# Kernel tuning notes

Hardware: AMD Instinct MI355X
Metric: run time of the kernel (lower is better)

The kernel has to match this reference:

```python
import jax, jax.numpy as jnp
import numpy as np

DIM = 512
HEAD_DIM = 32
NUM_HEADS = DIM // HEAD_DIM
SCALE = HEAD_DIM ** -0.5


def setup_inputs() -> dict:
    key = jax.random.key(0)
    k1, k2, k3 = jax.random.split(key, 3)
    B, H, W, C = 8, 32, 32, DIM
    x = jax.random.normal(k1, (B, H, W, C), dtype=jnp.float32)
    w_qkv = jax.random.normal(k2, (C, 3 * C), dtype=jnp.float32) * (C ** -0.5)
    w_proj = jax.random.normal(k3, (C, C), dtype=jnp.float32) * (C ** -0.5)
    b_proj = jnp.zeros((C,), dtype=jnp.float32)
    return {"x": x, "w_qkv": w_qkv, "w_proj": w_proj, "b_proj": b_proj}


def reference(x, w_qkv, w_proj, b_proj):
    B, H, W, C = x.shape
    N = H * W
    xt = x.reshape(B, N, C)
    qkv = xt @ w_qkv                       # [B, N, 3C]
    qkv = qkv.reshape(B, N, 3, NUM_HEADS, HEAD_DIM)
    qkv = jnp.transpose(qkv, (2, 0, 3, 1, 4))  # [3, B, heads, N, head_dim]
    q, k, v = qkv[0], qkv[1], qkv[2]
    attn = jnp.einsum('bhid,bhjd->bhij', q * SCALE, k)  # [B, heads, N, N]
    attn = jax.nn.softmax(attn, axis=-1)
    out = jnp.einsum('bhij,bhjd->bhid', attn, v)        # [B, heads, N, head_dim]
    out = jnp.transpose(out, (0, 2, 1, 3)).reshape(B, N, C)
    out = out @ w_proj + b_proj
    return out.reshape(B, H, W, C)
```

## Files before the change

### kernel.cpp

```cpp
#include <hip/hip_runtime.h>
#include <hip/hip_bf16.h>

typedef __bf16 bf16x8 __attribute__((ext_vector_type(8)));
typedef __bf16 bf16x4v __attribute__((ext_vector_type(4)));
typedef __bf16 bf16x2v __attribute__((ext_vector_type(2)));
typedef float  f32x4  __attribute__((ext_vector_type(4)));
typedef float  f32x16 __attribute__((ext_vector_type(16)));

#define NB 8
#define NTOK 1024
#define CDIM 512
#define NHEAD 16
#define HDIM 32
#define ATT_SCALE 0.17677669529663687f
#define LOG2E 1.4426950408889634f
#define QSCALE2 (ATT_SCALE * LOG2E)
#define NEGM2 (-12.0f * LOG2E)

struct __align__(8) bf4pack { __hip_bfloat16 x, y, z, w; };

__global__ __launch_bounds__(256)
void k_f32_to_bf16(const float* __restrict__ in, __hip_bfloat16* __restrict__ out, int n4) {
  int i = blockIdx.x * blockDim.x + threadIdx.x;
  if (i >= n4) return;
  float4 v = reinterpret_cast<const float4*>(in)[i];
  bf16x4v o = {(__bf16)v.x, (__bf16)v.y, (__bf16)v.z, (__bf16)v.w};
  reinterpret_cast<bf16x4v*>(out)[i] = o;
}

__global__ __launch_bounds__(256)
void k_transpose_bf16(const float* __restrict__ w, __hip_bfloat16* __restrict__ wt,
                      int K, int N) {
  __shared__ float tile[32][33];
  const int n0 = blockIdx.x * 32, k0 = blockIdx.y * 32;
  const int tx = threadIdx.x, ty = threadIdx.y;
  #pragma unroll
  for (int r = ty; r < 32; r += 8) tile[r][tx] = w[(size_t)(k0 + r) * N + n0 + tx];
  __syncthreads();
  #pragma unroll
  for (int r = ty; r < 32; r += 8)
    wt[(size_t)(n0 + r) * K + k0 + tx] = __float2bfloat16(tile[tx][r]);
}

__device__ __forceinline__ void gload_lds16(const void* g, void* l) {
  __builtin_amdgcn_global_load_lds(
      (const __attribute__((address_space(1))) unsigned int*)g,
      (__attribute__((address_space(3))) unsigned int*)l, 16, 0, 0);
}

template <int MODE>
__global__ __launch_bounds__(256, 2)
void gemm128(const __hip_bfloat16* __restrict__ A,
             const __hip_bfloat16* __restrict__ Bt,
             __hip_bfloat16* __restrict__ Qb,
             __hip_bfloat16* __restrict__ Kb,
             __hip_bfloat16* __restrict__ Vtb,
             float* __restrict__ outF,
             const float* __restrict__ bias,
             int mtiles, int ntiles) {
  __shared__ __hip_bfloat16 As[2][128 * 32];
  __shared__ __hip_bfloat16 Bs[2][128 * 32];

  const int t = threadIdx.x;
  const int wid = t >> 6, lane = t & 63;
  const int wr = wid >> 1, wc = wid & 1;
  const int lrow = lane & 15, lk8 = (lane >> 4) * 8;

  const int bid = blockIdx.x;
  const int chunk = (mtiles * ntiles) >> 3;
  const int wg = (bid & 7) * chunk + (bid >> 3);
  const int bm = (wg / ntiles) * 128;
  const int bn = (wg % ntiles) * 128;

  const bool swapped = (MODE == 1) || (bn < 1024);

  const f32x4 fzero = {0.f, 0.f, 0.f, 0.f};
  f32x4 acc[4][4];
  #pragma unroll
  for (int m = 0; m < 4; ++m)
    #pragma unroll
    for (int n = 0; n < 4; ++n) acc[m][n] = fzero;

  auto stage = [&](int buf, int kt) {
    #pragma unroll
    for (int p = 0; p < 2; ++p) {
      const int c = p * 256 + t;
      const int row = c >> 2;
      const int kof = (c & 3) * 8;
      gload_lds16(A + (size_t)(bm + row) * CDIM + kt * 32 + kof,
                  &As[buf][(p * 256 + (t >> 6) * 64) * 8]);
      gload_lds16(Bt + (size_t)(bn + row) * CDIM + kt * 32 + kof,
                  &Bs[buf][(p * 256 + (t >> 6) * 64) * 8]);
    }
  };

  stage(0, 0);
  const int NKT = CDIM / 32;
  for (int kt = 0; kt < NKT; ++kt) {
    __syncthreads();
    if (kt + 1 < NKT) stage((kt + 1) & 1, kt + 1);
    const int bi = kt & 1;
    bf16x8 af[4], bfv[4];
    #pragma unroll
    for (int m = 0; m < 4; ++m)
      af[m] = *reinterpret_cast<const bf16x8*>(&As[bi][(wr * 64 + m * 16 + lrow) * 32 + lk8]);
    #pragma unroll
    for (int n = 0; n < 4; ++n)
      bfv[n] = *reinterpret_cast<const bf16x8*>(&Bs[bi][(wc * 64 + n * 16 + lrow) * 32 + lk8]);
    if (swapped) {
      #pragma unroll
      for (int m = 0; m < 4; ++m)
        #pragma unroll
        for (int n = 0; n < 4; ++n)
          acc[m][n] = __builtin_amdgcn_mfma_f32_16x16x32_bf16(bfv[n], af[m], acc[m][n], 0, 0, 0);
    } else {
      #pragma unroll
      for (int m = 0; m < 4; ++m)
        #pragma unroll
        for (int n = 0; n < 4; ++n)
          acc[m][n] = __builtin_amdgcn_mfma_f32_16x16x32_bf16(af[m], bfv[n], acc[m][n], 0, 0, 0);
    }
  }

  if constexpr (MODE == 0) {
    if (swapped) {
      const float sc = (bn < 512) ? QSCALE2 : 1.0f;
      __hip_bfloat16* dst = (bn < 512) ? Qb : Kb;
      #pragma unroll
      for (int m = 0; m < 4; ++m) {
        #pragma unroll
        for (int n = 0; n < 4; ++n) {
          const int gm = bm + wr * 64 + m * 16 + lrow;
          const int gn0 = bn + wc * 64 + n * 16 + (lane >> 4) * 4;
          const int r = gn0 & 511;
          const int hh = r >> 5, d0 = r & 31;
          const int bb = gm >> 10, tok = gm & 1023;
          const int ph = bb * NHEAD + hh;
          bf16x4v pk = {(__bf16)(acc[m][n][0] * sc), (__bf16)(acc[m][n][1] * sc),
                        (__bf16)(acc[m][n][2] * sc), (__bf16)(acc[m][n][3] * sc)};
          *reinterpret_cast<bf16x4v*>(&dst[((size_t)ph * NTOK + tok) * HDIM + d0]) = pk;
        }
      }
    } else {
      #pragma unroll
      for (int m = 0; m < 4; ++m) {
        #pragma unroll
        for (int n = 0; n < 4; ++n) {
          const int gm0 = bm + wr * 64 + m * 16 + (lane >> 4) * 4;
          const int gn = bn + wc * 64 + n * 16 + lrow;
          const int r = gn & 511;
          const int hh = r >> 5, d = r & 31;
          const int bb = gm0 >> 10, tok0 = gm0 & 1023;
          const int ph = bb * NHEAD + hh;
          bf16x4v pk = {(__bf16)acc[m][n][0], (__bf16)acc[m][n][1],
                        (__bf16)acc[m][n][2], (__bf16)acc[m][n][3]};
          *reinterpret_cast<bf16x4v*>(&Vtb[((size_t)ph * HDIM + d) * NTOK + tok0]) = pk;
        }
      }
    }
  } else {
    float4 bias4[4];
    #pragma unroll
    for (int n = 0; n < 4; ++n)
      bias4[n] = *reinterpret_cast<const float4*>(&bias[bn + wc * 64 + n * 16 + (lane >> 4) * 4]);
    #pragma unroll
    for (int m = 0; m < 4; ++m) {
      #pragma unroll
      for (int n = 0; n < 4; ++n) {
        const int gm = bm + wr * 64 + m * 16 + lrow;
        const int gn0 = bn + wc * 64 + n * 16 + (lane >> 4) * 4;
        float4 w;
        w.x = acc[m][n][0] + bias4[n].x;
        w.y = acc[m][n][1] + bias4[n].y;
        w.z = acc[m][n][2] + bias4[n].z;
        w.w = acc[m][n][3] + bias4[n].w;
        *reinterpret_cast<float4*>(&outF[(size_t)gm * CDIM + gn0]) = w;
      }
    }
  }
}

__device__ __forceinline__ unsigned pk2(float a, float b) {
  bf16x2v t = {(__bf16)a, (__bf16)b};
  return __builtin_bit_cast(unsigned, t);
}

union B32x4 { unsigned u[4]; bf16x8 v; };

__global__ __launch_bounds__(256, 4)
void k_attn(const __hip_bfloat16* __restrict__ Q,
            const __hip_bfloat16* __restrict__ K,
            const __hip_bfloat16* __restrict__ Vt,
            __hip_bfloat16* __restrict__ out) {
  const int wid = threadIdx.x >> 6, lane = threadIdx.x & 63;
  const int pair = blockIdx.x & 127;
  const int qblk = blockIdx.x >> 7;
  const int b = pair >> 4, h = pair & 15;
  const int q0 = qblk * 128 + wid * 32;
  const int lq = lane & 31, hi = lane >> 5;

  const size_t pb = (size_t)pair * NTOK * HDIM;
  const bf16x8 qf0 = *reinterpret_cast<const bf16x8*>(&Q[pb + (size_t)(q0 + lq) * HDIM + hi * 8]);
  const bf16x8 qf1 = *reinterpret_cast<const bf16x8*>(&Q[pb + (size_t)(q0 + lq) * HDIM + 16 + hi * 8]);

  f32x16 o;
  #pragma unroll
  for (int r = 0; r < 16; ++r) o[r] = 0.f;
  float l_r = 0.f;

  const __hip_bfloat16* Kp = &K[pb + (size_t)lq * HDIM + hi * 8];
  const __hip_bfloat16* Vp = &Vt[(size_t)pair * HDIM * NTOK + (size_t)lq * NTOK + hi * 8];

  bf16x8 kc0 = *reinterpret_cast<const bf16x8*>(Kp);
  bf16x8 kc1 = *reinterpret_cast<const bf16x8*>(Kp + 16);

  for (int t = 0; t < 32; ++t) {
    const int tn = (t < 31) ? t + 1 : 31;
    const bf16x8 kn0 = *reinterpret_cast<const bf16x8*>(Kp + (size_t)tn * 32 * HDIM);
    const bf16x8 kn1 = *reinterpret_cast<const bf16x8*>(Kp + (size_t)tn * 32 * HDIM + 16);
    const bf16x8 vf0 = *reinterpret_cast<const bf16x8*>(Vp + t * 32);
    const bf16x8 vf1 = *reinterpret_cast<const bf16x8*>(Vp + t * 32 + 16);

    f32x16 s;
    #pragma unroll
    for (int r = 0; r < 16; ++r) s[r] = NEGM2;
    s = __builtin_amdgcn_mfma_f32_32x32x16_bf16(kc0, qf0, s, 0, 0, 0);
    s = __builtin_amdgcn_mfma_f32_32x32x16_bf16(kc1, qf1, s, 0, 0, 0);

    float p[16];
    #pragma unroll
    for (int r = 0; r < 16; ++r) p[r] = __builtin_amdgcn_exp2f(s[r]);
    {
      const float a0 = p[0] + p[1], a1 = p[2] + p[3], a2 = p[4] + p[5], a3 = p[6] + p[7];
      const float a4 = p[8] + p[9], a5 = p[10] + p[11], a6 = p[12] + p[13], a7 = p[14] + p[15];
      const float b0 = a0 + a1, b1 = a2 + a3, b2 = a4 + a5, b3 = a6 + a7;
      l_r += (b0 + b1) + (b2 + b3);
    }

    {
      unsigned pA = pk2(p[0], p[1]), pB = pk2(p[2], p[3]);
      unsigned pC = pk2(p[4], p[5]), pD = pk2(p[6], p[7]);
      asm("v_permlane32_swap_b32 %0, %1" : "+v"(pA), "+v"(pC));
      asm("v_permlane32_swap_b32 %0, %1" : "+v"(pB), "+v"(pD));
      B32x4 f; f.u[0] = pA; f.u[1] = pB; f.u[2] = pC; f.u[3] = pD;
      o = __builtin_amdgcn_mfma_f32_32x32x16_bf16(vf0, f.v, o, 0, 0, 0);
    }
    {
      unsigned pA = pk2(p[8], p[9]), pB = pk2(p[10], p[11]);
      unsigned pC = pk2(p[12], p[13]), pD = pk2(p[14], p[15]);
      asm("v_permlane32_swap_b32 %0, %1" : "+v"(pA), "+v"(pC));
      asm("v_permlane32_swap_b32 %0, %1" : "+v"(pB), "+v"(pD));
      B32x4 f; f.u[0] = pA; f.u[1] = pB; f.u[2] = pC; f.u[3] = pD;
      o = __builtin_amdgcn_mfma_f32_32x32x16_bf16(vf1, f.v, o, 0, 0, 0);
    }
    kc0 = kn0; kc1 = kn1;
  }

  l_r += __shfl_xor(l_r, 32, 64);
  const float rinv = 1.0f / l_r;
  __hip_bfloat16* orow = &out[((size_t)b * NTOK + q0 + lq) * CDIM + h * HDIM];
  #pragma unroll
  for (int g = 0; g < 4; ++g) {
    bf16x4v w = {(__bf16)(o[4 * g + 0] * rinv), (__bf16)(o[4 * g + 1] * rinv),
                 (__bf16)(o[4 * g + 2] * rinv), (__bf16)(o[4 * g + 3] * rinv)};
    *reinterpret_cast<bf16x4v*>(orow + 8 * g + 4 * hi) = w;
  }
}

extern "C" void kernel_launch(void* const* d_in, const int* in_sizes, int n_in,
                              void* d_out, int out_size, void* d_ws, size_t ws_size,
                              hipStream_t stream) {
  (void)in_sizes; (void)n_in; (void)out_size; (void)ws_size;
  const float* x      = (const float*)d_in[0];
  const float* w_qkv  = (const float*)d_in[1];
  const float* w_proj = (const float*)d_in[2];
  const float* b_proj = (const float*)d_in[3];
  float* out = (float*)d_out;

  char* ws = (char*)d_ws;
  __hip_bfloat16* xb     = (__hip_bfloat16*)(ws);
  __hip_bfloat16* attnO  = xb;
  __hip_bfloat16* wqkvT  = (__hip_bfloat16*)(ws + 8388608);
  __hip_bfloat16* wprojT = (__hip_bfloat16*)(ws + 9961472);
  __hip_bfloat16* Qb     = (__hip_bfloat16*)(ws + 10485760);
  __hip_bfloat16* Kb     = (__hip_bfloat16*)(ws + 18874368);
  __hip_bfloat16* Vtb    = (__hip_bfloat16*)(ws + 27262976);

  k_f32_to_bf16<<<4096, 256, 0, stream>>>(x, xb, (NB * NTOK * CDIM) / 4);
  k_transpose_bf16<<<dim3(1536 / 32, 512 / 32), dim3(32, 8), 0, stream>>>(w_qkv, wqkvT, 512, 1536);
  k_transpose_bf16<<<dim3(512 / 32, 512 / 32), dim3(32, 8), 0, stream>>>(w_proj, wprojT, 512, 512);

  gemm128<0><<<64 * 12, 256, 0, stream>>>(xb, wqkvT, Qb, Kb, Vtb, nullptr, nullptr, 64, 12);
  k_attn<<<128 * 8, 256, 0, stream>>>(Qb, Kb, Vtb, attnO);
  gemm128<1><<<64 * 4, 256, 0, stream>>>(attnO, wprojT, nullptr, nullptr, nullptr, out, b_proj, 64, 4);
}
```

Baseline: 169.0 us.

## Software-pipeline attention QK^T with exp and merge weight transposes into one launch

The attention loop is restructured so the QK^T MFMAs for the next key tile are issued before the exp2 and PV MFMAs of the current tile. K is prefetched two tiles ahead and V one ahead, with ping-pong register sets. This is meant to hide MFMA latency and the dependency between the score computation and the softmax/PV work. The two weight-transpose kernels are also fused into a single launch to save one kernel launch, at the cost of extra live registers in the attention kernel.

```diff
diff --git a/kernel.cpp b/kernel.cpp
--- a/kernel.cpp
+++ b/kernel.cpp
@@ -17,8 +17,6 @@
 #define QSCALE2 (ATT_SCALE * LOG2E)
 #define NEGM2 (-12.0f * LOG2E)
 
-struct __align__(8) bf4pack { __hip_bfloat16 x, y, z, w; };
-
 __global__ __launch_bounds__(256)
 void k_f32_to_bf16(const float* __restrict__ in, __hip_bfloat16* __restrict__ out, int n4) {
   int i = blockIdx.x * blockDim.x + threadIdx.x;
@@ -29,17 +27,22 @@
 }
 
 __global__ __launch_bounds__(256)
-void k_transpose_bf16(const float* __restrict__ w, __hip_bfloat16* __restrict__ wt,
-                      int K, int N) {
+void k_transpose_w(const float* __restrict__ wqkv, const float* __restrict__ wproj,
+                   __hip_bfloat16* __restrict__ wqkvT, __hip_bfloat16* __restrict__ wprojT) {
   __shared__ float tile[32][33];
   const int n0 = blockIdx.x * 32, k0 = blockIdx.y * 32;
   const int tx = threadIdx.x, ty = threadIdx.y;
-  #pragma unroll
-  for (int r = ty; r < 32; r += 8) tile[r][tx] = w[(size_t)(k0 + r) * N + n0 + tx];
+  const bool isP = (n0 >= 1536);
+  const float* src = isP ? wproj : wqkv;
+  __hip_bfloat16* dst = isP ? wprojT : wqkvT;
+  const int N = isP ? 512 : 1536;
+  const int nc = isP ? n0 - 1536 : n0;
+  #pragma unroll
+  for (int r = ty; r < 32; r += 8) tile[r][tx] = src[(size_t)(k0 + r) * N + nc + tx];
   __syncthreads();
   #pragma unroll
   for (int r = ty; r < 32; r += 8)
-    wt[(size_t)(n0 + r) * K + k0 + tx] = __float2bfloat16(tile[tx][r]);
+    dst[(size_t)(nc + r) * 512 + k0 + tx] = __float2bfloat16(tile[tx][r]);
 }
 
 __device__ __forceinline__ void gload_lds16(const void* g, void* l) {
@@ -203,57 +206,70 @@
   const bf16x8 qf0 = *reinterpret_cast<const bf16x8*>(&Q[pb + (size_t)(q0 + lq) * HDIM + hi * 8]);
   const bf16x8 qf1 = *reinterpret_cast<const bf16x8*>(&Q[pb + (size_t)(q0 + lq) * HDIM + 16 + hi * 8]);
 
-  f32x16 o;
-  #pragma unroll
-  for (int r = 0; r < 16; ++r) o[r] = 0.f;
+  f32x16 o, negm;
+  #pragma unroll
+  for (int r = 0; r < 16; ++r) { o[r] = 0.f; negm[r] = NEGM2; }
   float l_r = 0.f;
 
   const __hip_bfloat16* Kp = &K[pb + (size_t)lq * HDIM + hi * 8];
   const __hip_bfloat16* Vp = &Vt[(size_t)pair * HDIM * NTOK + (size_t)lq * NTOK + hi * 8];
 
-  bf16x8 kc0 = *reinterpret_cast<const bf16x8*>(Kp);
-  bf16x8 kc1 = *reinterpret_cast<const bf16x8*>(Kp + 16);
-
-  for (int t = 0; t < 32; ++t) {
-    const int tn = (t < 31) ? t + 1 : 31;
-    const bf16x8 kn0 = *reinterpret_cast<const bf16x8*>(Kp + (size_t)tn * 32 * HDIM);
-    const bf16x8 kn1 = *reinterpret_cast<const bf16x8*>(Kp + (size_t)tn * 32 * HDIM + 16);
-    const bf16x8 vf0 = *reinterpret_cast<const bf16x8*>(Vp + t * 32);
-    const bf16x8 vf1 = *reinterpret_cast<const bf16x8*>(Vp + t * 32 + 16);
-
-    f32x16 s;
-    #pragma unroll
-    for (int r = 0; r < 16; ++r) s[r] = NEGM2;
-    s = __builtin_amdgcn_mfma_f32_32x32x16_bf16(kc0, qf0, s, 0, 0, 0);
-    s = __builtin_amdgcn_mfma_f32_32x32x16_bf16(kc1, qf1, s, 0, 0, 0);
-
-    float p[16];
-    #pragma unroll
-    for (int r = 0; r < 16; ++r) p[r] = __builtin_amdgcn_exp2f(s[r]);
+  bf16x8 kA0, kA1, kB0, kB1, vA0, vA1, vB0, vB1;
+  f32x16 sA, sB;
+  {
+    const bf16x8 t0 = *reinterpret_cast<const bf16x8*>(Kp);
+    const bf16x8 t1 = *reinterpret_cast<const bf16x8*>(Kp + 16);
+    kA0 = *reinterpret_cast<const bf16x8*>(Kp + 1024);
+    kA1 = *reinterpret_cast<const bf16x8*>(Kp + 1024 + 16);
+    vA0 = *reinterpret_cast<const bf16x8*>(Vp);
+    vA1 = *reinterpret_cast<const bf16x8*>(Vp + 16);
+    sA = __builtin_amdgcn_mfma_f32_32x32x16_bf16(t0, qf0, negm, 0, 0, 0);
+    sA = __builtin_amdgcn_mfma_f32_32x32x16_bf16(t1, qf1, sA, 0, 0, 0);
+  }
+
+  auto body = [&](int t, f32x16& s_cur, f32x16& s_next,
+                  bf16x8& ka0, bf16x8& ka1, bf16x8& kb0, bf16x8& kb1,
+                  bf16x8& va0, bf16x8& va1, bf16x8& vb0, bf16x8& vb1) {
+    const int tk = (t + 2 < 32) ? t + 2 : 31;
+    const int tv = (t + 1 < 32) ? t + 1 : 31;
+    kb0 = *reinterpret_cast<const bf16x8*>(Kp + (size_t)tk * 1024);
+    kb1 = *reinterpret_cast<const bf16x8*>(Kp + (size_t)tk * 1024 + 16);
+    vb0 = *reinterpret_cast<const bf16x8*>(Vp + tv * 32);
+    vb1 = *reinterpret_cast<const bf16x8*>(Vp + tv * 32 + 16);
+
+    s_next = __builtin_amdgcn_mfma_f32_32x32x16_bf16(ka0, qf0, negm, 0, 0, 0);
+    s_next = __builtin_amdgcn_mfma_f32_32x32x16_bf16(ka1, qf1, s_next, 0, 0, 0);
+
+    #pragma unroll
+    for (int r = 0; r < 16; ++r) s_cur[r] = __builtin_amdgcn_exp2f(s_cur[r]);
     {
-      const float a0 = p[0] + p[1], a1 = p[2] + p[3], a2 = p[4] + p[5], a3 = p[6] + p[7];
-      const float a4 = p[8] + p[9], a5 = p[10] + p[11], a6 = p[12] + p[13], a7 = p[14] + p[15];
-      const float b0 = a0 + a1, b1 = a2 + a3, b2 = a4 + a5, b3 = a6 + a7;
-      l_r += (b0 + b1) + (b2 + b3);
-    }
-
+      const float a0 = s_cur[0] + s_cur[1], a1 = s_cur[2] + s_cur[3];
+      const float a2 = s_cur[4] + s_cur[5], a3 = s_cur[6] + s_cur[7];
+      const float a4 = s_cur[8] + s_cur[9], a5 = s_cur[10] + s_cur[11];
+      const float a6 = s_cur[12] + s_cur[13], a7 = s_cur[14] + s_cur[15];
+      l_r += ((a0 + a1) + (a2 + a3)) + ((a4 + a5) + (a6 + a7));
+    }
     {
-      unsigned pA = pk2(p[0], p[1]), pB = pk2(p[2], p[3]);
-      unsigned pC = pk2(p[4], p[5]), pD = pk2(p[6], p[7]);
+      unsigned pA = pk2(s_cur[0], s_cur[1]), pB = pk2(s_cur[2], s_cur[3]);
+      unsigned pC = pk2(s_cur[4], s_cur[5]), pD = pk2(s_cur[6], s_cur[7]);
       asm("v_permlane32_swap_b32 %0, %1" : "+v"(pA), "+v"(pC));
       asm("v_permlane32_swap_b32 %0, %1" : "+v"(pB), "+v"(pD));
       B32x4 f; f.u[0] = pA; f.u[1] = pB; f.u[2] = pC; f.u[3] = pD;
-      o = __builtin_amdgcn_mfma_f32_32x32x16_bf16(vf0, f.v, o, 0, 0, 0);
+      o = __builtin_amdgcn_mfma_f32_32x32x16_bf16(va0, f.v, o, 0, 0, 0);
     }
     {
-      unsigned pA = pk2(p[8], p[9]), pB = pk2(p[10], p[11]);
-      unsigned pC = pk2(p[12], p[13]), pD = pk2(p[14], p[15]);
+      unsigned pA = pk2(s_cur[8], s_cur[9]), pB = pk2(s_cur[10], s_cur[11]);
+      unsigned pC = pk2(s_cur[12], s_cur[13]), pD = pk2(s_cur[14], s_cur[15]);
       asm("v_permlane32_swap_b32 %0, %1" : "+v"(pA), "+v"(pC));
       asm("v_permlane32_swap_b32 %0, %1" : "+v"(pB), "+v"(pD));
       B32x4 f; f.u[0] = pA; f.u[1] = pB; f.u[2] = pC; f.u[3] = pD;
-      o = __builtin_amdgcn_mfma_f32_32x32x16_bf16(vf1, f.v, o, 0, 0, 0);
-    }
-    kc0 = kn0; kc1 = kn1;
+      o = __builtin_amdgcn_mfma_f32_32x32x16_bf16(va1, f.v, o, 0, 0, 0);
+    }
+  };
+
+  for (int t = 0; t < 32; t += 2) {
+    body(t,     sA, sB, kA0, kA1, kB0, kB1, vA0, vA1, vB0, vB1);
+    body(t + 1, sB, sA, kB0, kB1, kA0, kA1, vB0, vB1, vA0, vA1);
   }
 
   l_r += __shfl_xor(l_r, 32, 64);
@@ -287,8 +303,7 @@
   __hip_bfloat16* Vtb    = (__hip_bfloat16*)(ws + 27262976);
 
   k_f32_to_bf16<<<4096, 256, 0, stream>>>(x, xb, (NB * NTOK * CDIM) / 4);
-  k_transpose_bf16<<<dim3(1536 / 32, 512 / 32), dim3(32, 8), 0, stream>>>(w_qkv, wqkvT, 512, 1536);
-  k_transpose_bf16<<<dim3(512 / 32, 512 / 32), dim3(32, 8), 0, stream>>>(w_proj, wprojT, 512, 512);
+  k_transpose_w<<<dim3(64, 16), dim3(32, 8), 0, stream>>>(w_qkv, w_proj, wqkvT, wprojT);
 
   gemm128<0><<<64 * 12, 256, 0, stream>>>(xb, wqkvT, Qb, Kb, Vtb, nullptr, nullptr, 64, 12);
   k_attn<<<128 * 8, 256, 0, stream>>>(Qb, Kb, Vtb, attnO);
```

Measured after the change: 168.2 us. No clear change (-0.5%).

## Split attention key range across two wave groups and merge transposes

Applied to the files above, without the earlier changes.

The attention kernel now uses 512 threads per block. Each 32-query tile is handled by two waves, each covering half of the keys (512 tokens). The partial output accumulators and row sums from the second half are combined through shared memory before normalizing, which doubles the available wave-level parallelism and halves the serial loop length. The two weight-transpose launches are fused into one kernel to cut a launch. The kernel relies on the fixed max-subtraction constant, so the split needs no rescaling; the cost is extra LDS traffic and a block barrier.

```diff
diff --git a/kernel.cpp b/kernel.cpp
--- a/kernel.cpp
+++ b/kernel.cpp
@@ -17,8 +17,6 @@
 #define QSCALE2 (ATT_SCALE * LOG2E)
 #define NEGM2 (-12.0f * LOG2E)
 
-struct __align__(8) bf4pack { __hip_bfloat16 x, y, z, w; };
-
 __global__ __launch_bounds__(256)
 void k_f32_to_bf16(const float* __restrict__ in, __hip_bfloat16* __restrict__ out, int n4) {
   int i = blockIdx.x * blockDim.x + threadIdx.x;
@@ -29,17 +27,22 @@
 }
 
 __global__ __launch_bounds__(256)
-void k_transpose_bf16(const float* __restrict__ w, __hip_bfloat16* __restrict__ wt,
-                      int K, int N) {
+void k_transpose_w(const float* __restrict__ wqkv, const float* __restrict__ wproj,
+                   __hip_bfloat16* __restrict__ wqkvT, __hip_bfloat16* __restrict__ wprojT) {
   __shared__ float tile[32][33];
   const int n0 = blockIdx.x * 32, k0 = blockIdx.y * 32;
   const int tx = threadIdx.x, ty = threadIdx.y;
+  const bool isP = (n0 >= 1536);
+  const float* src = isP ? wproj : wqkv;
+  __hip_bfloat16* dst = isP ? wprojT : wqkvT;
+  const int N = isP ? 512 : 1536;
+  const int nc = isP ? n0 - 1536 : n0;
   #pragma unroll
-  for (int r = ty; r < 32; r += 8) tile[r][tx] = w[(size_t)(k0 + r) * N + n0 + tx];
+  for (int r = ty; r < 32; r += 8) tile[r][tx] = src[(size_t)(k0 + r) * N + nc + tx];
   __syncthreads();
   #pragma unroll
   for (int r = ty; r < 32; r += 8)
-    wt[(size_t)(n0 + r) * K + k0 + tx] = __float2bfloat16(tile[tx][r]);
+    dst[(size_t)(nc + r) * 512 + k0 + tx] = __float2bfloat16(tile[tx][r]);
 }
 
 __device__ __forceinline__ void gload_lds16(const void* g, void* l) {
@@ -187,67 +190,65 @@
 
 union B32x4 { unsigned u[4]; bf16x8 v; };
 
-__global__ __launch_bounds__(256, 4)
+__global__ __launch_bounds__(512, 8)
 void k_attn(const __hip_bfloat16* __restrict__ Q,
             const __hip_bfloat16* __restrict__ K,
             const __hip_bfloat16* __restrict__ Vt,
             __hip_bfloat16* __restrict__ out) {
-  const int wid = threadIdx.x >> 6, lane = threadIdx.x & 63;
+  __shared__ float Osh[4][64][17];
+  __shared__ float Lsh[4][64];
+  const int tid = threadIdx.x;
+  const int wid = tid >> 6, lane = tid & 63;
+  const int half = wid >> 2, wq = wid & 3;
   const int pair = blockIdx.x & 127;
   const int qblk = blockIdx.x >> 7;
   const int b = pair >> 4, h = pair & 15;
-  const int q0 = qblk * 128 + wid * 32;
+  const int q0 = qblk * 128 + wq * 32;
   const int lq = lane & 31, hi = lane >> 5;
 
   const size_t pb = (size_t)pair * NTOK * HDIM;
   const bf16x8 qf0 = *reinterpret_cast<const bf16x8*>(&Q[pb + (size_t)(q0 + lq) * HDIM + hi * 8]);
   const bf16x8 qf1 = *reinterpret_cast<const bf16x8*>(&Q[pb + (size_t)(q0 + lq) * HDIM + 16 + hi * 8]);
 
-  f32x16 o;
+  f32x16 o, negm;
   #pragma unroll
-  for (int r = 0; r < 16; ++r) o[r] = 0.f;
+  for (int r = 0; r < 16; ++r) { o[r] = 0.f; negm[r] = NEGM2; }
   float l_r = 0.f;
 
-  const __hip_bfloat16* Kp = &K[pb + (size_t)lq * HDIM + hi * 8];
-  const __hip_bfloat16* Vp = &Vt[(size_t)pair * HDIM * NTOK + (size_t)lq * NTOK + hi * 8];
+  const __hip_bfloat16* Kp = &K[pb + (size_t)(half * 512 + lq) * HDIM + hi * 8];
+  const __hip_bfloat16* Vp = &Vt[(size_t)pair * HDIM * NTOK + (size_t)lq * NTOK + half * 512 + hi * 8];
 
   bf16x8 kc0 = *reinterpret_cast<const bf16x8*>(Kp);
   bf16x8 kc1 = *reinterpret_cast<const bf16x8*>(Kp + 16);
 
-  for (int t = 0; t < 32; ++t) {
-    const int tn = (t < 31) ? t + 1 : 31;
-    const bf16x8 kn0 = *reinterpret_cast<const bf16x8*>(Kp + (size_t)tn * 32 * HDIM);
-    const bf16x8 kn1 = *reinterpret_cast<const bf16x8*>(Kp + (size_t)tn * 32 * HDIM + 16);
+  for (int t = 0; t < 16; ++t) {
+    const int tn = (t < 15) ? t + 1 : 15;
+    const bf16x8 kn0 = *reinterpret_cast<const bf16x8*>(Kp + (size_t)tn * 1024);
+    const bf16x8 kn1 = *reinterpret_cast<const bf16x8*>(Kp + (size_t)tn * 1024 + 16);
     const bf16x8 vf0 = *reinterpret_cast<const bf16x8*>(Vp + t * 32);
     const bf16x8 vf1 = *reinterpret_cast<const bf16x8*>(Vp + t * 32 + 16);
 
-    f32x16 s;
-    #pragma unroll
-    for (int r = 0; r < 16; ++r) s[r] = NEGM2;
-    s = __builtin_amdgcn_mfma_f32_32x32x16_bf16(kc0, qf0, s, 0, 0, 0);
+    f32x16 s = __builtin_amdgcn_mfma_f32_32x32x16_bf16(kc0, qf0, negm, 0, 0, 0);
     s = __builtin_amdgcn_mfma_f32_32x32x16_bf16(kc1, qf1, s, 0, 0, 0);
 
-    float p[16];
-    #pragma unroll
-    for (int r = 0; r < 16; ++r) p[r] = __builtin_amdgcn_exp2f(s[r]);
+    #pragma unroll
+    for (int r = 0; r < 16; ++r) s[r] = __builtin_amdgcn_exp2f(s[r]);
     {
-      const float a0 = p[0] + p[1], a1 = p[2] + p[3], a2 = p[4] + p[5], a3 = p[6] + p[7];
-      const float a4 = p[8] + p[9], a5 = p[10] + p[11], a6 = p[12] + p[13], a7 = p[14] + p[15];
-      const float b0 = a0 + a1, b1 = a2 + a3, b2 = a4 + a5, b3 = a6 + a7;
-      l_r += (b0 + b1) + (b2 + b3);
-    }
-
+      const float a0 = s[0] + s[1], a1 = s[2] + s[3], a2 = s[4] + s[5], a3 = s[6] + s[7];
+      const float a4 = s[8] + s[9], a5 = s[10] + s[11], a6 = s[12] + s[13], a7 = s[14] + s[15];
+      l_r += ((a0 + a1) + (a2 + a3)) + ((a4 + a5) + (a6 + a7));
+    }
     {
-      unsigned pA = pk2(p[0], p[1]), pB = pk2(p[2], p[3]);
-      unsigned pC = pk2(p[4], p[5]), pD = pk2(p[6], p[7]);
+      unsigned pA = pk2(s[0], s[1]), pB = pk2(s[2], s[3]);
+      unsigned pC = pk2(s[4], s[5]), pD = pk2(s[6], s[7]);
       asm("v_permlane32_swap_b32 %0, %1" : "+v"(pA), "+v"(pC));
       asm("v_permlane32_swap_b32 %0, %1" : "+v"(pB), "+v"(pD));
       B32x4 f; f.u[0] = pA; f.u[1] = pB; f.u[2] = pC; f.u[3] = pD;
       o = __builtin_amdgcn_mfma_f32_32x32x16_bf16(vf0, f.v, o, 0, 0, 0);
     }
     {
-      unsigned pA = pk2(p[8], p[9]), pB = pk2(p[10], p[11]);
-      unsigned pC = pk2(p[12], p[13]), pD = pk2(p[14], p[15]);
+      unsigned pA = pk2(s[8], s[9]), pB = pk2(s[10], s[11]);
+      unsigned pC = pk2(s[12], s[13]), pD = pk2(s[14], s[15]);
       asm("v_permlane32_swap_b32 %0, %1" : "+v"(pA), "+v"(pC));
       asm("v_permlane32_swap_b32 %0, %1" : "+v"(pB), "+v"(pD));
       B32x4 f; f.u[0] = pA; f.u[1] = pB; f.u[2] = pC; f.u[3] = pD;
@@ -256,14 +257,25 @@
     kc0 = kn0; kc1 = kn1;
   }
 
-  l_r += __shfl_xor(l_r, 32, 64);
-  const float rinv = 1.0f / l_r;
-  __hip_bfloat16* orow = &out[((size_t)b * NTOK + q0 + lq) * CDIM + h * HDIM];
-  #pragma unroll
-  for (int g = 0; g < 4; ++g) {
-    bf16x4v w = {(__bf16)(o[4 * g + 0] * rinv), (__bf16)(o[4 * g + 1] * rinv),
-                 (__bf16)(o[4 * g + 2] * rinv), (__bf16)(o[4 * g + 3] * rinv)};
-    *reinterpret_cast<bf16x4v*>(orow + 8 * g + 4 * hi) = w;
+  if (half) {
+    #pragma unroll
+    for (int r = 0; r < 16; ++r) Osh[wq][lane][r] = o[r];
+    Lsh[wq][lane] = l_r;
+  }
+  __syncthreads();
+  if (!half) {
+    #pragma unroll
+    for (int r = 0; r < 16; ++r) o[r] += Osh[wq][lane][r];
+    l_r += Lsh[wq][lane];
+    l_r += __shfl_xor(l_r, 32, 64);
+    const float rinv = 1.0f / l_r;
+    __hip_bfloat16* orow = &out[((size_t)b * NTOK + q0 + lq) * CDIM + h * HDIM];
+    #pragma unroll
+    for (int g = 0; g < 4; ++g) {
+      bf16x4v w = {(__bf16)(o[4 * g + 0] * rinv), (__bf16)(o[4 * g + 1] * rinv),
+                   (__bf16)(o[4 * g + 2] * rinv), (__bf16)(o[4 * g + 3] * rinv)};
+      *reinterpret_cast<bf16x4v*>(orow + 8 * g + 4 * hi) = w;
+    }
   }
 }
 
@@ -287,10 +299,9 @@
   __hip_bfloat16* Vtb    = (__hip_bfloat16*)(ws + 27262976);
 
   k_f32_to_bf16<<<4096, 256, 0, stream>>>(x, xb, (NB * NTOK * CDIM) / 4);
-  k_transpose_bf16<<<dim3(1536 / 32, 512 / 32), dim3(32, 8), 0, stream>>>(w_qkv, wqkvT, 512, 1536);
-  k_transpose_bf16<<<dim3(512 / 32, 512 / 32), dim3(32, 8), 0, stream>>>(w_proj, wprojT, 512, 512);
+  k_transpose_w<<<dim3(64, 16), dim3(32, 8), 0, stream>>>(w_qkv, w_proj, wqkvT, wprojT);
 
   gemm128<0><<<64 * 12, 256, 0, stream>>>(xb, wqkvT, Qb, Kb, Vtb, nullptr, nullptr, 64, 12);
-  k_attn<<<128 * 8, 256, 0, stream>>>(Qb, Kb, Vtb, attnO);
+  k_attn<<<128 * 8, 512, 0, stream>>>(Qb, Kb, Vtb, attnO);
   gemm128<1><<<64 * 4, 256, 0, stream>>>(attnO, wprojT, nullptr, nullptr, nullptr, out, b_proj, 64, 4);
 }
```

Result: slower. 257.7 us (+52.4%).
